# Optimization experiments

Measured on AMD Instinct MI355X. Metric: run time of the kernel, lower is better.

## Reference

```python
import jax, jax.numpy as jnp
import numpy as np
import math

# Fixed rendering constants (from module-level source)
FOV_X = 60.0
FOV_Y = 60.0
NEAR = 0.1
FAR = 10000.0
SCALE_MODIFIER = 1.0
MAX_FREQUENCY = 128.0
NUM_TOTAL_FREQUENCIES = 1024
GAUSSIAN_ONLY = False
COV_DILATION = 0.3  # low-pass dilation as in 3DGS EWA splatting

N_PRIM = 512
TOP_K = 8
IMG_H = 200
IMG_W = 200


def _quat_to_rotmat(q):
    # q: [N,4] (r, x, y, z), normalized
    q = q / (jnp.linalg.norm(q, axis=-1, keepdims=True) + 1e-8)
    r, x, y, z = q[:, 0], q[:, 1], q[:, 2], q[:, 3]
    R = jnp.stack([
        jnp.stack([1 - 2 * (y * y + z * z), 2 * (x * y - r * z), 2 * (x * z + r * y)], -1),
        jnp.stack([2 * (x * y + r * z), 1 - 2 * (x * x + z * z), 2 * (y * z - r * x)], -1),
        jnp.stack([2 * (x * z - r * y), 2 * (y * z + r * x), 1 - 2 * (x * x + y * y)], -1),
    ], axis=-2)  # [N,3,3]
    return R


def _forward(colors, opacities, background_color, positions, scales, rotations,
             topk_wave_coefficients, topk_wave_indices, cam_position,
             view_matrix, VP_matrix, image_width, image_height):
    H, W = image_height, image_width
    N = positions.shape[0]
    tan_x = math.tan(math.radians(FOV_X * 0.5))
    tan_y = math.tan(math.radians(FOV_Y * 0.5))
    fx = W / (2.0 * tan_x)
    fy = H / (2.0 * tan_y)

    # --- 3D covariance: Sigma = R diag(s^2) R^T, s = exp(log_scales) * modifier
    R = _quat_to_rotmat(rotations)                     # [N,3,3]
    s = jnp.exp(scales) * SCALE_MODIFIER               # [N,3]
    Sigma = jnp.einsum('nij,nj,nkj->nik', R, s * s, R)  # [N,3,3]

    # --- projection
    p_hom = jnp.concatenate([positions, jnp.ones((N, 1), positions.dtype)], -1)  # [N,4]
    t_cam = jnp.einsum('ij,nj->ni', view_matrix, p_hom)[:, :3]                   # [N,3] camera space
    clip = jnp.einsum('ij,nj->ni', VP_matrix, p_hom)                             # [N,4]
    wclip = clip[:, 3:4]
    ndc = clip[:, :2] / jnp.where(jnp.abs(wclip) > 1e-6, wclip, 1e-6)
    px = (ndc * 0.5 + 0.5) * jnp.array([W, H], positions.dtype)                  # [N,2] pixel center
    depth = t_cam[:, 2]

    # --- EWA 2D covariance: cov2d = J Wr Sigma Wr^T J^T + dilation
    tz = jnp.maximum(depth, NEAR)
    tx, ty = t_cam[:, 0], t_cam[:, 1]
    zeros = jnp.zeros_like(tz)
    J = jnp.stack([
        jnp.stack([fx / tz, zeros, -fx * tx / (tz * tz)], -1),
        jnp.stack([zeros, fy / tz, -fy * ty / (tz * tz)], -1),
    ], axis=-2)                                         # [N,2,3]
    Wr = view_matrix[:3, :3]
    M = jnp.einsum('nij,jk->nik', J, Wr)                # [N,2,3]
    cov2d = jnp.einsum('nab,nbc,ndc->nad', M, Sigma, M) # [N,2,2]
    A = cov2d[:, 0, 0] + COV_DILATION
    B = cov2d[:, 0, 1]
    C = cov2d[:, 1, 1] + COV_DILATION
    det = jnp.maximum(A * C - B * B, 1e-12)
    conA, conB, conC = C / det, -B / det, A / det       # conic (inverse cov)

    # --- pixel grid [H*W]
    ys = jnp.arange(H, dtype=positions.dtype) + 0.5
    xs = jnp.arange(W, dtype=positions.dtype) + 0.5
    gy, gx = jnp.meshgrid(ys, xs, indexing='ij')
    gx, gy = gx.ravel(), gy.ravel()

    dx = px[:, 0:1] - gx[None, :]                       # [N,HW]
    dy = px[:, 1:2] - gy[None, :]
    power = -0.5 * (conA[:, None] * dx * dx + conC[:, None] * dy * dy) - conB[:, None] * dx * dy
    G = jnp.exp(jnp.minimum(power, 0.0))                # [N,HW]

    # --- periodic (Gabor) modulation along projected primary axis of each primitive
    if GAUSSIAN_ONLY:
        wave = 1.0
    else:
        a3 = R[:, :, 0]                                  # local first axis, world space [N,3]
        a2 = jnp.einsum('nij,nj->ni', M, a3)             # projected to screen [N,2]
        a2 = a2 / (jnp.linalg.norm(a2, axis=-1, keepdims=True) + 1e-8)
        tcoord = (dx * a2[:, 0:1] + dy * a2[:, 1:2]) / W  # [N,HW], normalized coord
        freqs = topk_wave_indices.astype(positions.dtype) * (MAX_FREQUENCY / NUM_TOTAL_FREQUENCIES)  # [N,K]
        wave = jnp.zeros_like(tcoord)
        for k in range(topk_wave_indices.shape[1]):      # small fixed K, unrolled
            wave = wave + topk_wave_coefficients[:, k:k + 1] * jnp.cos(
                2.0 * jnp.pi * freqs[:, k:k + 1] * tcoord)

    alpha = jnp.clip(opacities * G * wave, 0.0, 0.99)   # [N,HW]
    valid = (depth > NEAR) & (wclip[:, 0] > 1e-4)
    alpha = jnp.where(valid[:, None], alpha, 0.0)

    # --- depth sort + front-to-back alpha compositing
    order = jnp.argsort(depth)
    alpha_s = alpha[order]
    colors_s = colors[order]
    Tprod = jnp.cumprod(1.0 - alpha_s, axis=0)           # inclusive transmittance
    T_excl = jnp.concatenate([jnp.ones((1, alpha_s.shape[1]), alpha_s.dtype), Tprod[:-1]], 0)
    img = jnp.einsum('nc,np->cp', colors_s, alpha_s * T_excl)  # [3,HW]
    img = img + background_color[:, None] * Tprod[-1][None, :]
    return img.reshape(3, H, W)


def setup_inputs() -> dict:
    key = jax.random.key(0)
    ks = jax.random.split(key, 10)
    N, K = N_PRIM, TOP_K
    colors = jax.random.uniform(ks[0], (N, 3), jnp.float32)
    opacities = 0.8 * jax.random.uniform(ks[1], (N, 1), jnp.float32)
    background_color = jnp.zeros((3,), jnp.float32)
    # positions inside the view frustum: z in [4,12], xy in [-3,3]
    xy = jax.random.uniform(ks[2], (N, 2), jnp.float32, -3.0, 3.0)
    z = jax.random.uniform(ks[3], (N, 1), jnp.float32, 4.0, 12.0)
    positions = jnp.concatenate([xy, z], -1)
    scales = -2.5 + 0.3 * jax.random.normal(ks[4], (N, 3), jnp.float32)  # log-scales
    rotations = jax.random.normal(ks[5], (N, 4), jnp.float32)
    topk_wave_coefficients = 0.1 * jax.random.normal(ks[6], (N, K), jnp.float32)
    topk_wave_indices = jax.random.randint(ks[7], (N, K), 1, NUM_TOTAL_FREQUENCIES).astype(jnp.int32)
    cam_position = jnp.zeros((3,), jnp.float32)
    view_matrix = jnp.eye(4, dtype=jnp.float32)
    tan_x = math.tan(math.radians(FOV_X * 0.5))
    tan_y = math.tan(math.radians(FOV_Y * 0.5))
    P = jnp.array([[1.0 / tan_x, 0, 0, 0],
                   [0, 1.0 / tan_y, 0, 0],
                   [0, 0, FAR / (FAR - NEAR), -FAR * NEAR / (FAR - NEAR)],
                   [0, 0, 1.0, 0]], jnp.float32)
    VP_matrix = P @ view_matrix
    return {
        'colors': colors, 'opacities': opacities, 'background_color': background_color,
        'positions': positions, 'scales': scales, 'rotations': rotations,
        'topk_wave_coefficients': topk_wave_coefficients, 'topk_wave_indices': topk_wave_indices,
        'cam_position': cam_position, 'view_matrix': view_matrix, 'VP_matrix': VP_matrix,
        'image_width': IMG_W, 'image_height': IMG_H,
    }


def reference(colors, opacities, background_color, positions, scales, rotations,
              topk_wave_coefficients, topk_wave_indices, cam_position,
              view_matrix, VP_matrix, image_width, image_height):
    return _forward(colors, opacities, background_color, positions, scales, rotations,
                    topk_wave_coefficients, topk_wave_indices, cam_position,
                    view_matrix, VP_matrix, image_width, image_height)
```

## Files before the change

### kernel.cpp

```cpp
#include <hip/hip_runtime.h>
#include <math.h>

#define NPRIM   512
#define TOPK    8
#define PSTRIDE 28
#define IMG     200
#define NPIX    (IMG * IMG)
#define NSEG    8
#define SEGSZ   (NPRIM / NSEG)
#define TILE    64
#define TILES_X (IMG / 8)


__global__ __launch_bounds__(NPRIM) void prep_kernel(
    const float* __restrict__ colors,
    const float* __restrict__ opacities,
    const float* __restrict__ positions,
    const float* __restrict__ scales,
    const float* __restrict__ rotations,
    const float* __restrict__ wcoef,
    const int*   __restrict__ widx,
    const float* __restrict__ view,
    const float* __restrict__ VP,
    float* __restrict__ table,
    float4* __restrict__ bbox)
{
    const int n = threadIdx.x;
    const float tanx = 0.57735026918962576451f;
    const float fx = IMG / (2.0f * tanx);
    const float fy = IMG / (2.0f * tanx);

    float qr = rotations[n*4+0], qx = rotations[n*4+1];
    float qy = rotations[n*4+2], qz = rotations[n*4+3];
    float qn = sqrtf(qr*qr + qx*qx + qy*qy + qz*qz) + 1e-8f;
    qr /= qn; qx /= qn; qy /= qn; qz /= qn;
    float R00 = 1.f - 2.f*(qy*qy + qz*qz), R01 = 2.f*(qx*qy - qr*qz), R02 = 2.f*(qx*qz + qr*qy);
    float R10 = 2.f*(qx*qy + qr*qz), R11 = 1.f - 2.f*(qx*qx + qz*qz), R12 = 2.f*(qy*qz - qr*qx);
    float R20 = 2.f*(qx*qz - qr*qy), R21 = 2.f*(qy*qz + qr*qx), R22 = 1.f - 2.f*(qx*qx + qy*qy);

    float s0 = expf(scales[n*3+0]); s0 *= s0;
    float s1 = expf(scales[n*3+1]); s1 *= s1;
    float s2 = expf(scales[n*3+2]); s2 *= s2;

    float S00 = R00*R00*s0 + R01*R01*s1 + R02*R02*s2;
    float S01 = R00*R10*s0 + R01*R11*s1 + R02*R12*s2;
    float S02 = R00*R20*s0 + R01*R21*s1 + R02*R22*s2;
    float S11 = R10*R10*s0 + R11*R11*s1 + R12*R12*s2;
    float S12 = R10*R20*s0 + R11*R21*s1 + R12*R22*s2;
    float S22 = R20*R20*s0 + R21*R21*s1 + R22*R22*s2;

    float px_ = positions[n*3+0], py_ = positions[n*3+1], pz_ = positions[n*3+2];
    float t0 = view[0]*px_ + view[1]*py_ + view[2]*pz_  + view[3];
    float t1 = view[4]*px_ + view[5]*py_ + view[6]*pz_  + view[7];
    float t2 = view[8]*px_ + view[9]*py_ + view[10]*pz_ + view[11];
    float c0 = VP[0]*px_  + VP[1]*py_  + VP[2]*pz_  + VP[3];
    float c1 = VP[4]*px_  + VP[5]*py_  + VP[6]*pz_  + VP[7];
    float w  = VP[12]*px_ + VP[13]*py_ + VP[14]*pz_ + VP[15];

    float denom = (fabsf(w) > 1e-6f) ? w : 1e-6f;
    float pxs = (c0/denom * 0.5f + 0.5f) * (float)IMG;
    float pys = (c1/denom * 0.5f + 0.5f) * (float)IMG;

    float depth = t2;
    float tz = fmaxf(depth, 0.1f);
    float invz = 1.f / tz;
    float J00 = fx*invz, J02 = -fx*t0*invz*invz;
    float J11 = fy*invz, J12 = -fy*t1*invz*invz;

    float M00 = J00*view[0] + J02*view[8];
    float M01 = J00*view[1] + J02*view[9];
    float M02 = J00*view[2] + J02*view[10];
    float M10 = J11*view[4] + J12*view[8];
    float M11 = J11*view[5] + J12*view[9];
    float M12 = J11*view[6] + J12*view[10];

    float T00 = M00*S00 + M01*S01 + M02*S02;
    float T01 = M00*S01 + M01*S11 + M02*S12;
    float T02 = M00*S02 + M01*S12 + M02*S22;
    float T10 = M10*S00 + M11*S01 + M12*S02;
    float T11 = M10*S01 + M11*S11 + M12*S12;
    float T12 = M10*S02 + M11*S12 + M12*S22;
    float cA = T00*M00 + T01*M01 + T02*M02 + 0.3f;
    float cB = T00*M10 + T01*M11 + T02*M12;
    float cC = T10*M10 + T11*M11 + T12*M12 + 0.3f;
    float det  = fmaxf(cA*cC - cB*cB, 1e-12f);
    float idet = 1.f / det;
    float conA = cC*idet, conB = -cB*idet, conC = cA*idet;

    float a2x = M00*R00 + M01*R10 + M02*R20;
    float a2y = M10*R00 + M11*R10 + M12*R20;
    float an = sqrtf(a2x*a2x + a2y*a2y) + 1e-8f;
    a2x = (a2x/an) * (1.0f/(float)IMG);
    a2y = (a2y/an) * (1.0f/(float)IMG);

    bool valid = (depth > 0.1f) && (w > 1e-4f);
    float op = valid ? opacities[n] : 0.0f;

    float rx = valid ? sqrtf(fmaxf(30.f * cA, 0.f)) : -1e30f;
    float ry = valid ? sqrtf(fmaxf(30.f * cC, 0.f)) : -1e30f;

    __shared__ float sd[NPRIM];
    sd[n] = depth;
    __syncthreads();
    int rank = 0;
#pragma unroll 8
    for (int m = 0; m < NPRIM; ++m) {
        float dm = sd[m];
        rank += (dm < depth) || (dm == depth && m < n);
    }

    float* e = table + rank * PSTRIDE;
    e[0]=pxs; e[1]=pys; e[2]=conA; e[3]=conB; e[4]=conC;
    e[5]=a2x; e[6]=a2y; e[7]=op;
    e[8]=colors[n*3+0]; e[9]=colors[n*3+1]; e[10]=colors[n*3+2]; e[11]=0.f;
#pragma unroll
    for (int k = 0; k < TOPK; ++k) {
        e[12+k] = wcoef[n*TOPK+k];
        e[20+k] = 0.78539816339744830962f * (float)widx[n*TOPK+k];
    }
    bbox[rank] = make_float4(pxs, pys, rx, ry);
}

__global__ __launch_bounds__(NSEG*64, 4) void render_kernel(
    const float*  __restrict__ table,
    const float4* __restrict__ bbox,
    const float*  __restrict__ bg,
    float* __restrict__ out)
{
    __shared__ float  lds[NPRIM * PSTRIDE];
    __shared__ float4 part[NSEG * TILE];

    const int lane = threadIdx.x & 63;
    const int wv   = threadIdx.x >> 6;
    const int tx   = blockIdx.x % TILES_X, ty = blockIdx.x / TILES_X;
    const int x    = tx*8 + (lane & 7);
    const int y    = ty*8 + (lane >> 3);
    const float gx = (float)x + 0.5f, gy = (float)y + 0.5f;

    {
        const float4* src = (const float4*)table + wv * (SEGSZ * PSTRIDE / 4);
        float4*       dst = (float4*)lds         + wv * (SEGSZ * PSTRIDE / 4);
#pragma unroll
        for (int q = 0; q < 7; ++q) dst[q*64 + lane] = src[q*64 + lane];
    }

    const float tcx = (float)(tx*8) + 4.0f, tcy = (float)(ty*8) + 4.0f;
    float4 bb = bbox[wv * SEGSZ + lane];
    bool active = (fabsf(bb.x - tcx) <= bb.z + 3.5f) &&
                  (fabsf(bb.y - tcy) <= bb.w + 3.5f);
    unsigned long long mask = __ballot(active);

    float T = 1.f, cr = 0.f, cg = 0.f, cb = 0.f;
    const float* seg = lds + (wv * SEGSZ) * PSTRIDE;
    while (mask) {
        int j = __ffsll((unsigned long long)mask) - 1;
        mask &= mask - 1;
        const float* h = seg + j * PSTRIDE;
        float4 q0 = *(const float4*)(h);
        float4 q1 = *(const float4*)(h + 4);
        float dx = q0.x - gx, dy = q0.y - gy;
        float pw = -0.5f*(q0.z*dx*dx + q1.x*dy*dy) - q0.w*dx*dy;
        if (__any(pw > -15.0f)) {
            float4 q2 = *(const float4*)(h + 8);
            float4 c0 = *(const float4*)(h + 12), c1 = *(const float4*)(h + 16);
            float4 w0 = *(const float4*)(h + 20), w1 = *(const float4*)(h + 24);
            float G = __expf(fminf(pw, 0.f));
            float t = dx*q1.y + dy*q1.z;
            float wave = c0.x*__cosf(w0.x*t) + c0.y*__cosf(w0.y*t)
                       + c0.z*__cosf(w0.z*t) + c0.w*__cosf(w0.w*t)
                       + c1.x*__cosf(w1.x*t) + c1.y*__cosf(w1.y*t)
                       + c1.z*__cosf(w1.z*t) + c1.w*__cosf(w1.w*t);
            float a = fminf(fmaxf(q1.w * G * wave, 0.f), 0.99f);
            float wgt = a * T;
            cr += q2.x*wgt; cg += q2.y*wgt; cb += q2.z*wgt;
            T *= (1.f - a);
        }
    }
    part[wv*TILE + lane] = make_float4(cr, cg, cb, T);

    __syncthreads();

    if (threadIdx.x < TILE) {
        float Ta = 1.f, fr = 0.f, fg = 0.f, fb = 0.f;
#pragma unroll
        for (int s = 0; s < NSEG; ++s) {
            float4 v = part[s*TILE + lane];
            fr += Ta * v.x; fg += Ta * v.y; fb += Ta * v.z;
            Ta *= v.w;
        }
        const int p = y*IMG + x;
        out[p]          = fr + bg[0]*Ta;
        out[NPIX + p]   = fg + bg[1]*Ta;
        out[2*NPIX + p] = fb + bg[2]*Ta;
    }
}

extern "C" void kernel_launch(void* const* d_in, const int* in_sizes, int n_in,
                              void* d_out, int out_size, void* d_ws, size_t ws_size,
                              hipStream_t stream) {
    const float* colors  = (const float*)d_in[0];
    const float* opac    = (const float*)d_in[1];
    const float* bg      = (const float*)d_in[2];
    const float* pos     = (const float*)d_in[3];
    const float* scales  = (const float*)d_in[4];
    const float* rot     = (const float*)d_in[5];
    const float* wcoef   = (const float*)d_in[6];
    const int*   widx    = (const int*)d_in[7];
    const float* view    = (const float*)d_in[9];
    const float* VP      = (const float*)d_in[10];

    float*  table = (float*)d_ws;
    float4* bbox  = (float4*)((char*)d_ws + NPRIM * PSTRIDE * sizeof(float));

    hipLaunchKernelGGL(prep_kernel, dim3(1), dim3(NPRIM), 0, stream,
                       colors, opac, pos, scales, rot, wcoef, widx, view, VP,
                       table, bbox);
    hipLaunchKernelGGL(render_kernel, dim3(TILES_X*TILES_X), dim3(NSEG*64), 0, stream,
                       table, bbox, bg, (float*)d_out);
}
```

Measured before the change: 94.67 us.

## Fuse preprocessing into render kernel with persistent tile loop

Merges the single-block prep kernel and the tiled render kernel into one launch. Each of the 209 blocks redundantly computes the per-primitive projection, covariance and depth sort straight into shared memory, then loops over 625 tiles in a grid-stride fashion. This removes the second launch, the global table round trip and the serial dependency on a one-block kernel. In exchange every block repeats the O(N^2) rank sort and the setup math, and each tile iteration adds an extra barrier.

```diff
diff --git a/kernel.cpp b/kernel.cpp
--- a/kernel.cpp
+++ b/kernel.cpp
@@ -10,9 +10,11 @@
 #define SEGSZ   (NPRIM / NSEG)
 #define TILE    64
 #define TILES_X (IMG / 8)
-
-
-__global__ __launch_bounds__(NPRIM) void prep_kernel(
+#define NTILES  (TILES_X * TILES_X)
+#define GRID    209
+
+
+__global__ __launch_bounds__(NPRIM) void fused_kernel(
     const float* __restrict__ colors,
     const float* __restrict__ opacities,
     const float* __restrict__ positions,
@@ -22,176 +24,172 @@
     const int*   __restrict__ widx,
     const float* __restrict__ view,
     const float* __restrict__ VP,
-    float* __restrict__ table,
-    float4* __restrict__ bbox)
-{
-    const int n = threadIdx.x;
-    const float tanx = 0.57735026918962576451f;
-    const float fx = IMG / (2.0f * tanx);
-    const float fy = IMG / (2.0f * tanx);
-
-    float qr = rotations[n*4+0], qx = rotations[n*4+1];
-    float qy = rotations[n*4+2], qz = rotations[n*4+3];
-    float qn = sqrtf(qr*qr + qx*qx + qy*qy + qz*qz) + 1e-8f;
-    qr /= qn; qx /= qn; qy /= qn; qz /= qn;
-    float R00 = 1.f - 2.f*(qy*qy + qz*qz), R01 = 2.f*(qx*qy - qr*qz), R02 = 2.f*(qx*qz + qr*qy);
-    float R10 = 2.f*(qx*qy + qr*qz), R11 = 1.f - 2.f*(qx*qx + qz*qz), R12 = 2.f*(qy*qz - qr*qx);
-    float R20 = 2.f*(qx*qz - qr*qy), R21 = 2.f*(qy*qz + qr*qx), R22 = 1.f - 2.f*(qx*qx + qy*qy);
-
-    float s0 = expf(scales[n*3+0]); s0 *= s0;
-    float s1 = expf(scales[n*3+1]); s1 *= s1;
-    float s2 = expf(scales[n*3+2]); s2 *= s2;
-
-    float S00 = R00*R00*s0 + R01*R01*s1 + R02*R02*s2;
-    float S01 = R00*R10*s0 + R01*R11*s1 + R02*R12*s2;
-    float S02 = R00*R20*s0 + R01*R21*s1 + R02*R22*s2;
-    float S11 = R10*R10*s0 + R11*R11*s1 + R12*R12*s2;
-    float S12 = R10*R20*s0 + R11*R21*s1 + R12*R22*s2;
-    float S22 = R20*R20*s0 + R21*R21*s1 + R22*R22*s2;
-
-    float px_ = positions[n*3+0], py_ = positions[n*3+1], pz_ = positions[n*3+2];
-    float t0 = view[0]*px_ + view[1]*py_ + view[2]*pz_  + view[3];
-    float t1 = view[4]*px_ + view[5]*py_ + view[6]*pz_  + view[7];
-    float t2 = view[8]*px_ + view[9]*py_ + view[10]*pz_ + view[11];
-    float c0 = VP[0]*px_  + VP[1]*py_  + VP[2]*pz_  + VP[3];
-    float c1 = VP[4]*px_  + VP[5]*py_  + VP[6]*pz_  + VP[7];
-    float w  = VP[12]*px_ + VP[13]*py_ + VP[14]*pz_ + VP[15];
-
-    float denom = (fabsf(w) > 1e-6f) ? w : 1e-6f;
-    float pxs = (c0/denom * 0.5f + 0.5f) * (float)IMG;
-    float pys = (c1/denom * 0.5f + 0.5f) * (float)IMG;
-
-    float depth = t2;
-    float tz = fmaxf(depth, 0.1f);
-    float invz = 1.f / tz;
-    float J00 = fx*invz, J02 = -fx*t0*invz*invz;
-    float J11 = fy*invz, J12 = -fy*t1*invz*invz;
-
-    float M00 = J00*view[0] + J02*view[8];
-    float M01 = J00*view[1] + J02*view[9];
-    float M02 = J00*view[2] + J02*view[10];
-    float M10 = J11*view[4] + J12*view[8];
-    float M11 = J11*view[5] + J12*view[9];
-    float M12 = J11*view[6] + J12*view[10];
-
-    float T00 = M00*S00 + M01*S01 + M02*S02;
-    float T01 = M00*S01 + M01*S11 + M02*S12;
-    float T02 = M00*S02 + M01*S12 + M02*S22;
-    float T10 = M10*S00 + M11*S01 + M12*S02;
-    float T11 = M10*S01 + M11*S11 + M12*S12;
-    float T12 = M10*S02 + M11*S12 + M12*S22;
-    float cA = T00*M00 + T01*M01 + T02*M02 + 0.3f;
-    float cB = T00*M10 + T01*M11 + T02*M12;
-    float cC = T10*M10 + T11*M11 + T12*M12 + 0.3f;
-    float det  = fmaxf(cA*cC - cB*cB, 1e-12f);
-    float idet = 1.f / det;
-    float conA = cC*idet, conB = -cB*idet, conC = cA*idet;
-
-    float a2x = M00*R00 + M01*R10 + M02*R20;
-    float a2y = M10*R00 + M11*R10 + M12*R20;
-    float an = sqrtf(a2x*a2x + a2y*a2y) + 1e-8f;
-    a2x = (a2x/an) * (1.0f/(float)IMG);
-    a2y = (a2y/an) * (1.0f/(float)IMG);
-
-    bool valid = (depth > 0.1f) && (w > 1e-4f);
-    float op = valid ? opacities[n] : 0.0f;
-
-    float rx = valid ? sqrtf(fmaxf(30.f * cA, 0.f)) : -1e30f;
-    float ry = valid ? sqrtf(fmaxf(30.f * cC, 0.f)) : -1e30f;
-
-    __shared__ float sd[NPRIM];
-    sd[n] = depth;
-    __syncthreads();
-    int rank = 0;
-#pragma unroll 8
-    for (int m = 0; m < NPRIM; ++m) {
-        float dm = sd[m];
-        rank += (dm < depth) || (dm == depth && m < n);
-    }
-
-    float* e = table + rank * PSTRIDE;
-    e[0]=pxs; e[1]=pys; e[2]=conA; e[3]=conB; e[4]=conC;
-    e[5]=a2x; e[6]=a2y; e[7]=op;
-    e[8]=colors[n*3+0]; e[9]=colors[n*3+1]; e[10]=colors[n*3+2]; e[11]=0.f;
-#pragma unroll
-    for (int k = 0; k < TOPK; ++k) {
-        e[12+k] = wcoef[n*TOPK+k];
-        e[20+k] = 0.78539816339744830962f * (float)widx[n*TOPK+k];
-    }
-    bbox[rank] = make_float4(pxs, pys, rx, ry);
-}
-
-__global__ __launch_bounds__(NSEG*64, 4) void render_kernel(
-    const float*  __restrict__ table,
-    const float4* __restrict__ bbox,
-    const float*  __restrict__ bg,
+    const float* __restrict__ bg,
     float* __restrict__ out)
 {
     __shared__ float  lds[NPRIM * PSTRIDE];
+    __shared__ float4 sbb[NPRIM];
     __shared__ float4 part[NSEG * TILE];
-
-    const int lane = threadIdx.x & 63;
-    const int wv   = threadIdx.x >> 6;
-    const int tx   = blockIdx.x % TILES_X, ty = blockIdx.x / TILES_X;
-    const int x    = tx*8 + (lane & 7);
-    const int y    = ty*8 + (lane >> 3);
-    const float gx = (float)x + 0.5f, gy = (float)y + 0.5f;
+    __shared__ float  sd[NPRIM];
+
+    const int n = threadIdx.x;
 
     {
-        const float4* src = (const float4*)table + wv * (SEGSZ * PSTRIDE / 4);
-        float4*       dst = (float4*)lds         + wv * (SEGSZ * PSTRIDE / 4);
+        const float tanx = 0.57735026918962576451f;
+        const float fx = IMG / (2.0f * tanx);
+        const float fy = IMG / (2.0f * tanx);
+
+        float qr = rotations[n*4+0], qx = rotations[n*4+1];
+        float qy = rotations[n*4+2], qz = rotations[n*4+3];
+        float qn = sqrtf(qr*qr + qx*qx + qy*qy + qz*qz) + 1e-8f;
+        qr /= qn; qx /= qn; qy /= qn; qz /= qn;
+        float R00 = 1.f - 2.f*(qy*qy + qz*qz), R01 = 2.f*(qx*qy - qr*qz), R02 = 2.f*(qx*qz + qr*qy);
+        float R10 = 2.f*(qx*qy + qr*qz), R11 = 1.f - 2.f*(qx*qx + qz*qz), R12 = 2.f*(qy*qz - qr*qx);
+        float R20 = 2.f*(qx*qz - qr*qy), R21 = 2.f*(qy*qz + qr*qx), R22 = 1.f - 2.f*(qx*qx + qy*qy);
+
+        float s0 = expf(scales[n*3+0]); s0 *= s0;
+        float s1 = expf(scales[n*3+1]); s1 *= s1;
+        float s2 = expf(scales[n*3+2]); s2 *= s2;
+
+        float S00 = R00*R00*s0 + R01*R01*s1 + R02*R02*s2;
+        float S01 = R00*R10*s0 + R01*R11*s1 + R02*R12*s2;
+        float S02 = R00*R20*s0 + R01*R21*s1 + R02*R22*s2;
+        float S11 = R10*R10*s0 + R11*R11*s1 + R12*R12*s2;
+        float S12 = R10*R20*s0 + R11*R21*s1 + R12*R22*s2;
+        float S22 = R20*R20*s0 + R21*R21*s1 + R22*R22*s2;
+
+        float px_ = positions[n*3+0], py_ = positions[n*3+1], pz_ = positions[n*3+2];
+        float t0 = view[0]*px_ + view[1]*py_ + view[2]*pz_  + view[3];
+        float t1 = view[4]*px_ + view[5]*py_ + view[6]*pz_  + view[7];
+        float t2 = view[8]*px_ + view[9]*py_ + view[10]*pz_ + view[11];
+        float c0 = VP[0]*px_  + VP[1]*py_  + VP[2]*pz_  + VP[3];
+        float c1 = VP[4]*px_  + VP[5]*py_  + VP[6]*pz_  + VP[7];
+        float w  = VP[12]*px_ + VP[13]*py_ + VP[14]*pz_ + VP[15];
+
+        float denom = (fabsf(w) > 1e-6f) ? w : 1e-6f;
+        float pxs = (c0/denom * 0.5f + 0.5f) * (float)IMG;
+        float pys = (c1/denom * 0.5f + 0.5f) * (float)IMG;
+
+        float depth = t2;
+        float tz = fmaxf(depth, 0.1f);
+        float invz = 1.f / tz;
+        float J00 = fx*invz, J02 = -fx*t0*invz*invz;
+        float J11 = fy*invz, J12 = -fy*t1*invz*invz;
+
+        float M00 = J00*view[0] + J02*view[8];
+        float M01 = J00*view[1] + J02*view[9];
+        float M02 = J00*view[2] + J02*view[10];
+        float M10 = J11*view[4] + J12*view[8];
+        float M11 = J11*view[5] + J12*view[9];
+        float M12 = J11*view[6] + J12*view[10];
+
+        float T00 = M00*S00 + M01*S01 + M02*S02;
+        float T01 = M00*S01 + M01*S11 + M02*S12;
+        float T02 = M00*S02 + M01*S12 + M02*S22;
+        float T10 = M10*S00 + M11*S01 + M12*S02;
+        float T11 = M10*S01 + M11*S11 + M12*S12;
+        float T12 = M10*S02 + M11*S12 + M12*S22;
+        float cA = T00*M00 + T01*M01 + T02*M02 + 0.3f;
+        float cB = T00*M10 + T01*M11 + T02*M12;
+        float cC = T10*M10 + T11*M11 + T12*M12 + 0.3f;
+        float det  = fmaxf(cA*cC - cB*cB, 1e-12f);
+        float idet = 1.f / det;
+        float conA = cC*idet, conB = -cB*idet, conC = cA*idet;
+
+        float a2x = M00*R00 + M01*R10 + M02*R20;
+        float a2y = M10*R00 + M11*R10 + M12*R20;
+        float an = sqrtf(a2x*a2x + a2y*a2y) + 1e-8f;
+        a2x = (a2x/an) * (1.0f/(float)IMG);
+        a2y = (a2y/an) * (1.0f/(float)IMG);
+
+        bool valid = (depth > 0.1f) && (w > 1e-4f);
+        float op = valid ? opacities[n] : 0.0f;
+
+        float rx = valid ? sqrtf(fmaxf(30.f * cA, 0.f)) : -1e30f;
+        float ry = valid ? sqrtf(fmaxf(30.f * cC, 0.f)) : -1e30f;
+
+        sd[n] = depth;
+        __syncthreads();
+        int rank = 0;
+#pragma unroll 8
+        for (int m = 0; m < NPRIM; ++m) {
+            float dm = sd[m];
+            rank += (dm < depth) || (dm == depth && m < n);
+        }
+
+        float* e = lds + rank * PSTRIDE;
+        e[0]=pxs; e[1]=pys; e[2]=conA; e[3]=conB; e[4]=conC;
+        e[5]=a2x; e[6]=a2y; e[7]=op;
+        e[8]=colors[n*3+0]; e[9]=colors[n*3+1]; e[10]=colors[n*3+2]; e[11]=0.f;
 #pragma unroll
-        for (int q = 0; q < 7; ++q) dst[q*64 + lane] = src[q*64 + lane];
+        for (int k = 0; k < TOPK; ++k) {
+            e[12+k] = wcoef[n*TOPK+k];
+            e[20+k] = 0.78539816339744830962f * (float)widx[n*TOPK+k];
+        }
+        sbb[rank] = make_float4(pxs, pys, rx, ry);
     }
-
-    const float tcx = (float)(tx*8) + 4.0f, tcy = (float)(ty*8) + 4.0f;
-    float4 bb = bbox[wv * SEGSZ + lane];
-    bool active = (fabsf(bb.x - tcx) <= bb.z + 3.5f) &&
-                  (fabsf(bb.y - tcy) <= bb.w + 3.5f);
-    unsigned long long mask = __ballot(active);
-
-    float T = 1.f, cr = 0.f, cg = 0.f, cb = 0.f;
+    __syncthreads();
+
+    const int lane = n & 63;
+    const int wv   = n >> 6;
+    const float4 bb = sbb[wv * SEGSZ + lane];
     const float* seg = lds + (wv * SEGSZ) * PSTRIDE;
-    while (mask) {
-        int j = __ffsll((unsigned long long)mask) - 1;
-        mask &= mask - 1;
-        const float* h = seg + j * PSTRIDE;
-        float4 q0 = *(const float4*)(h);
-        float4 q1 = *(const float4*)(h + 4);
-        float dx = q0.x - gx, dy = q0.y - gy;
-        float pw = -0.5f*(q0.z*dx*dx + q1.x*dy*dy) - q0.w*dx*dy;
-        if (__any(pw > -15.0f)) {
-            float4 q2 = *(const float4*)(h + 8);
-            float4 c0 = *(const float4*)(h + 12), c1 = *(const float4*)(h + 16);
-            float4 w0 = *(const float4*)(h + 20), w1 = *(const float4*)(h + 24);
-            float G = __expf(fminf(pw, 0.f));
-            float t = dx*q1.y + dy*q1.z;
-            float wave = c0.x*__cosf(w0.x*t) + c0.y*__cosf(w0.y*t)
-                       + c0.z*__cosf(w0.z*t) + c0.w*__cosf(w0.w*t)
-                       + c1.x*__cosf(w1.x*t) + c1.y*__cosf(w1.y*t)
-                       + c1.z*__cosf(w1.z*t) + c1.w*__cosf(w1.w*t);
-            float a = fminf(fmaxf(q1.w * G * wave, 0.f), 0.99f);
-            float wgt = a * T;
-            cr += q2.x*wgt; cg += q2.y*wgt; cb += q2.z*wgt;
-            T *= (1.f - a);
-        }
-    }
-    part[wv*TILE + lane] = make_float4(cr, cg, cb, T);
-
-    __syncthreads();
-
-    if (threadIdx.x < TILE) {
-        float Ta = 1.f, fr = 0.f, fg = 0.f, fb = 0.f;
+    const float bg0 = bg[0], bg1 = bg[1], bg2 = bg[2];
+
+    for (int t = blockIdx.x; t < NTILES; t += GRID) {
+        const int tx = t % TILES_X, ty = t / TILES_X;
+        const int x  = tx*8 + (lane & 7);
+        const int y  = ty*8 + (lane >> 3);
+        const float gx = (float)x + 0.5f, gy = (float)y + 0.5f;
+
+        const float tcx = (float)(tx*8) + 4.0f, tcy = (float)(ty*8) + 4.0f;
+        bool active = (fabsf(bb.x - tcx) <= bb.z + 3.5f) &&
+                      (fabsf(bb.y - tcy) <= bb.w + 3.5f);
+        unsigned long long mask = __ballot(active);
+
+        float T = 1.f, cr = 0.f, cg = 0.f, cb = 0.f;
+        while (mask) {
+            int j = __ffsll((unsigned long long)mask) - 1;
+            mask &= mask - 1;
+            const float* h = seg + j * PSTRIDE;
+            float4 q0 = *(const float4*)(h);
+            float4 q1 = *(const float4*)(h + 4);
+            float dx = q0.x - gx, dy = q0.y - gy;
+            float pw = -0.5f*(q0.z*dx*dx + q1.x*dy*dy) - q0.w*dx*dy;
+            if (__any(pw > -15.0f)) {
+                float4 q2 = *(const float4*)(h + 8);
+                float4 c0 = *(const float4*)(h + 12), c1 = *(const float4*)(h + 16);
+                float4 w0 = *(const float4*)(h + 20), w1 = *(const float4*)(h + 24);
+                float G = __expf(fminf(pw, 0.f));
+                float tt = dx*q1.y + dy*q1.z;
+                float wave = c0.x*__cosf(w0.x*tt) + c0.y*__cosf(w0.y*tt)
+                           + c0.z*__cosf(w0.z*tt) + c0.w*__cosf(w0.w*tt)
+                           + c1.x*__cosf(w1.x*tt) + c1.y*__cosf(w1.y*tt)
+                           + c1.z*__cosf(w1.z*tt) + c1.w*__cosf(w1.w*tt);
+                float a = fminf(fmaxf(q1.w * G * wave, 0.f), 0.99f);
+                float wgt = a * T;
+                cr += q2.x*wgt; cg += q2.y*wgt; cb += q2.z*wgt;
+                T *= (1.f - a);
+            }
+        }
+        part[wv*TILE + lane] = make_float4(cr, cg, cb, T);
+
+        __syncthreads();
+
+        if (n < TILE) {
+            float Ta = 1.f, fr = 0.f, fg = 0.f, fb = 0.f;
 #pragma unroll
-        for (int s = 0; s < NSEG; ++s) {
-            float4 v = part[s*TILE + lane];
-            fr += Ta * v.x; fg += Ta * v.y; fb += Ta * v.z;
-            Ta *= v.w;
-        }
-        const int p = y*IMG + x;
-        out[p]          = fr + bg[0]*Ta;
-        out[NPIX + p]   = fg + bg[1]*Ta;
-        out[2*NPIX + p] = fb + bg[2]*Ta;
+            for (int s = 0; s < NSEG; ++s) {
+                float4 v = part[s*TILE + lane];
+                fr += Ta * v.x; fg += Ta * v.y; fb += Ta * v.z;
+                Ta *= v.w;
+            }
+            const int p = y*IMG + x;
+            out[p]          = fr + bg0*Ta;
+            out[NPIX + p]   = fg + bg1*Ta;
+            out[2*NPIX + p] = fb + bg2*Ta;
+        }
+        __syncthreads();
     }
 }
 
@@ -209,12 +207,7 @@
     const float* view    = (const float*)d_in[9];
     const float* VP      = (const float*)d_in[10];
 
-    float*  table = (float*)d_ws;
-    float4* bbox  = (float4*)((char*)d_ws + NPRIM * PSTRIDE * sizeof(float));
-
-    hipLaunchKernelGGL(prep_kernel, dim3(1), dim3(NPRIM), 0, stream,
+    hipLaunchKernelGGL(fused_kernel, dim3(GRID), dim3(NPRIM), 0, stream,
                        colors, opac, pos, scales, rot, wcoef, widx, view, VP,
-                       table, bbox);
-    hipLaunchKernelGGL(render_kernel, dim3(TILES_X*TILES_X), dim3(NSEG*64), 0, stream,
-                       table, bbox, bg, (float*)d_out);
+                       bg, (float*)d_out);
 }
```

Measured after the change: 98.78 us. 4.3% more time.
